# Performance work log

Measured on AMD Instinct MI355X. Metric: run time of the kernel, lower is better.

## Reference

```python
import jax, jax.numpy as jnp
import numpy as np

B, NL, C, H, W = 4, 2048, 128, 128, 128
N_PTS0, N_PTS1 = 32, 8
SCALE = N_PTS0 // N_PTS1  # MaxPool1d kernel/stride
FEATURE_DIM = 5
BN_EPS = 1e-5


def setup_inputs() -> dict:
    key = jax.random.key(0)
    ks = jax.random.split(key, 12)
    fm = jax.random.normal(ks[0], (B, C, H, W), dtype=jnp.float32)
    lines = jax.random.uniform(ks[1], (B, NL, 2, 2), dtype=jnp.float32) * 128.0
    P = C // 2
    s = 0.05
    return {
        "feature_map": fm,
        "lines": lines,
        # Bottleneck1D params (BatchNorm in eval mode: running_mean=0, running_var=1)
        "bn1_g": jnp.ones((C,), jnp.float32), "bn1_b": jnp.zeros((C,), jnp.float32),
        "conv1_w": jax.random.normal(ks[2], (P, C, 1), jnp.float32) * s,
        "conv1_b": jnp.zeros((P,), jnp.float32),
        "bn2_g": jnp.ones((P,), jnp.float32), "bn2_b": jnp.zeros((P,), jnp.float32),
        "conv2_w": jax.random.normal(ks[3], (P, P, 3), jnp.float32) * s,
        "conv2_b": jnp.zeros((P,), jnp.float32),
        "bn3_g": jnp.ones((P,), jnp.float32), "bn3_b": jnp.zeros((P,), jnp.float32),
        "conv3_w": jax.random.normal(ks[4], (C, P, 1), jnp.float32) * s,
        "conv3_b": jnp.zeros((C,), jnp.float32),
        # fc2: ReLU -> Linear(dim_loi*n_pts1 + 5, 4)
        "fc2_w": jax.random.normal(ks[5], (4, C * N_PTS1 + FEATURE_DIM), jnp.float32) * s,
        "fc2_b": jnp.zeros((4,), jnp.float32),
    }


def _bn(x, g, b):
    # eval-mode BatchNorm1d with running_mean=0, running_var=1
    return x * (g / jnp.sqrt(1.0 + BN_EPS))[None, :, None] + b[None, :, None]


def _conv1d(x, w, b, pad):
    y = jax.lax.conv_general_dilated(x, w, (1,), [(pad, pad)],
                                     dimension_numbers=("NCH", "OIH", "NCH"))
    return y + b[None, :, None]


def _loi_gather(fm, lines):
    # sample points along each line: [B, NL, N_PTS0, 2]
    lam = jnp.linspace(0.0, 1.0, N_PTS0, dtype=jnp.float32)[None, None, :, None]
    p = lines[:, :, 0:1, :] * lam + lines[:, :, 1:2, :] * (1.0 - lam) - 0.5
    p = p.reshape(B, -1, 2)                      # [B, NL*N_PTS0, 2]
    px, py = p[..., 0], p[..., 1]
    px0 = jnp.clip(jnp.floor(px), 0.0, 127.0)
    py0 = jnp.clip(jnp.floor(py), 0.0, 127.0)
    px1 = jnp.clip(px0 + 1.0, 0.0, 127.0)
    py1 = jnp.clip(py0 + 1.0, 0.0, 127.0)
    px0l, py0l = px0.astype(jnp.int32), py0.astype(jnp.int32)
    px1l, py1l = px1.astype(jnp.int32), py1.astype(jnp.int32)

    gather = jax.vmap(lambda f, yi, xi: f[:, yi, xi])  # [C, P] per image
    # weights exactly as in the torch source
    xp = (gather(fm, py0l, px0l) * ((px1 - px) * (py1 - py))[:, None, :]
          + gather(fm, py1l, px0l) * ((px - px0) * (py1 - py))[:, None, :]
          + gather(fm, py0l, px1l) * ((px1 - px) * (py - py0))[:, None, :]
          + gather(fm, py1l, px1l) * ((px - px0) * (py - py0))[:, None, :])
    # [B, C, NL*N_PTS0] -> [B*NL, C, N_PTS0]
    xp = xp.reshape(B, C, NL, N_PTS0).transpose(0, 2, 1, 3).reshape(B * NL, C, N_PTS0)
    return xp


def reference(feature_map, lines, bn1_g, bn1_b, conv1_w, conv1_b,
              bn2_g, bn2_b, conv2_w, conv2_b, bn3_g, bn3_b,
              conv3_w, conv3_b, fc2_w, fc2_b):
    xp = _loi_gather(feature_map, lines)               # [B*NL, C, N_PTS0]
    # MaxPool1d(SCALE, SCALE)
    x = xp.reshape(B * NL, C, N_PTS1, SCALE).max(axis=-1)
    # Bottleneck1D residual block
    y = jax.nn.relu(_bn(x, bn1_g, bn1_b))
    y = _conv1d(y, conv1_w, conv1_b, 0)
    y = jax.nn.relu(_bn(y, bn2_g, bn2_b))
    y = _conv1d(y, conv2_w, conv2_b, 1)
    y = jax.nn.relu(_bn(y, bn3_g, bn3_b))
    y = _conv1d(y, conv3_w, conv3_b, 0)
    x = x + y                                          # [B*NL, C, N_PTS1]
    # line geometry feature (use_cood=1, use_slop=1)
    xyu, xyv = lines[:, :, 0, :], lines[:, :, 1, :]
    u2v = jnp.sqrt(((xyu - xyv) ** 2).sum(-1, keepdims=True)).clip(min=1e-6)
    f = jnp.concatenate([xyu / 128.0, xyv / 128.0, u2v], axis=-1)
    f = f.reshape(B * NL, FEATURE_DIM)
    # concat + fc2 (ReLU -> Linear)
    x = jnp.concatenate([x.reshape(B * NL, C * N_PTS1), f], axis=1)
    logits = jax.nn.relu(x) @ fc2_w.T + fc2_b
    prob = jax.nn.softmax(logits, axis=1)
    return logits, prob
```

## Files before the change

### kernel.cpp

```cpp
#include <hip/hip_runtime.h>
#include <math.h>

#define BB 4
#define NLL 2048
#define CC 128
#define HH 128
#define WW 128
#define NPTS0 32
#define NPTS1 8
#define PP 64
#define FDIM 5
#define FCK (CC*NPTS1 + FDIM)
#define FCKP 1032

typedef __attribute__((ext_vector_type(8))) short bf16x8;
typedef __attribute__((ext_vector_type(4))) float f32x4;

__device__ __forceinline__ unsigned short f2bf(float f) {
    union { float f; unsigned u; } v; v.f = f;
    unsigned u = v.u;
    return (unsigned short)((u + 0x7fffu + ((u >> 16) & 1u)) >> 16);
}
__device__ __forceinline__ float bf2f(unsigned short s) {
    union { unsigned u; float f; } v; v.u = ((unsigned)s) << 16;
    return v.f;
}

__global__ __launch_bounds__(256)
void transpose_prep(const float* __restrict__ fm, const float* __restrict__ w1,
                    const float* __restrict__ w2, const float* __restrict__ w3,
                    const float* __restrict__ fcw,
                    unsigned short* __restrict__ fmT,
                    unsigned short* __restrict__ W1b,
                    unsigned short* __restrict__ W2b,
                    unsigned short* __restrict__ W3b,
                    float* __restrict__ fcwP) {
    const int t = threadIdx.x;
    if (blockIdx.x >= 512) {
        int gid = (blockIdx.x - 512) * 256 + t;
        for (int e = gid; e < 32800; e += 4096) {
            if (e < 8192) {
                W1b[e] = f2bf(w1[e]);
            } else if (e < 20480) {
                int g = e - 8192;
                int tt = g >> 12, r = g & 4095;
                int p = r >> 6, q = r & 63;
                W2b[tt * 4096 + p * 64 + q] = f2bf(w2[p * 192 + q * 3 + tt]);
            } else if (e < 28672) {
                int g = e - 20480;
                W3b[g] = f2bf(w3[g]);
            } else {
                int g = e - 28672;
                int o = g / FCKP, r = g - o * FCKP;
                fcwP[g] = (r < FCK) ? fcw[o * FCK + r] : 0.0f;
            }
        }
        return;
    }
    __shared__ unsigned short tile[2][128 * 72];
    const int by = blockIdx.x;
    const int b = by >> 7, y = by & 127;
    const float* src = fm + ((size_t)b * CC) * (HH * WW) + (size_t)y * WW;
    const int x4 = (t & 31) * 4;
    const int xh = x4 >> 6, xl = x4 & 63;
    #pragma unroll
    for (int i = 0; i < 16; ++i) {
        int r = (t >> 5) + 8 * i;
        float4 v = *(const float4*)&src[(size_t)r * (HH * WW) + x4];
        ushort4 u;
        u.x = f2bf(v.x); u.y = f2bf(v.y); u.z = f2bf(v.z); u.w = f2bf(v.w);
        *(ushort4*)&tile[xh][r * 72 + (xl ^ (r & 28))] = u;
    }
    __syncthreads();
    const int c4 = (t & 31) * 4;
    #pragma unroll
    for (int h = 0; h < 2; ++h) {
        unsigned short* dst = fmT + ((size_t)by * WW + h * 64) * CC;
        #pragma unroll
        for (int i = 0; i < 8; ++i) {
            int x = (t >> 5) + 8 * i;
            ushort4 u;
            u.x = tile[h][(c4 + 0) * 72 + (x ^ ((c4 + 0) & 28))];
            u.y = tile[h][(c4 + 1) * 72 + (x ^ ((c4 + 1) & 28))];
            u.z = tile[h][(c4 + 2) * 72 + (x ^ ((c4 + 2) & 28))];
            u.w = tile[h][(c4 + 3) * 72 + (x ^ ((c4 + 3) & 28))];
            *(ushort4*)&dst[(size_t)x * CC + c4] = u;
        }
    }
}

__global__ __launch_bounds__(256, 8)
void line_mfma(const unsigned short* __restrict__ fmT,
               const float* __restrict__ lines,
               const float* __restrict__ bn1_g, const float* __restrict__ bn1_b,
               const unsigned short* __restrict__ W1b, const float* __restrict__ b1,
               const float* __restrict__ bn2_g, const float* __restrict__ bn2_b,
               const unsigned short* __restrict__ W2b, const float* __restrict__ b2,
               const float* __restrict__ bn3_g, const float* __restrict__ bn3_b,
               const unsigned short* __restrict__ W3b, const float* __restrict__ b3,
               const float* __restrict__ fcwP,  const float* __restrict__ fcb,
               float* __restrict__ out) {
    __shared__ int   s_oA[64], s_oB[64], s_oC[64], s_oD[64];
    __shared__ float s_wA[64], s_wB[64], s_wC[64], s_wD[64];
    __shared__ float s_xs[16 * 132];
    __shared__ unsigned short s_ybn[16 * 136];
    __shared__ unsigned short s_z1[2 * 10 * 72];
    __shared__ unsigned short s_z2[16 * 72];
    __shared__ float s_feat[2][8];
    __shared__ float s_red[4 * 8];

    const int bx  = blockIdx.x;
    const int L0  = bx * 2;
    const int b   = bx >> 10;
    const int tid = threadIdx.x;
    const int lane = tid & 63;
    const int wv   = tid >> 6;
    const int quad = lane >> 4;
    const int l16  = lane & 15;
    const float inv_s = 1.0f / sqrtf(1.0f + 1e-5f);

    if (tid < 64) {
        int line = tid >> 5, pt = tid & 31;
        const float* ln = lines + (size_t)(L0 + line) * 4;
        float lam = (float)pt * (1.0f / 31.0f);
        float om  = 1.0f - lam;
        float px = ln[0] * lam + ln[2] * om - 0.5f;
        float py = ln[1] * lam + ln[3] * om - 0.5f;
        float px0 = fminf(fmaxf(floorf(px), 0.0f), 127.0f);
        float py0 = fminf(fmaxf(floorf(py), 0.0f), 127.0f);
        float px1 = fminf(px0 + 1.0f, 127.0f);
        float py1 = fminf(py0 + 1.0f, 127.0f);
        int ix0 = (int)px0, ix1 = (int)px1, iy0 = (int)py0, iy1 = (int)py1;
        s_oA[tid] = (iy0 * WW + ix0) * CC;
        s_oB[tid] = (iy1 * WW + ix0) * CC;
        s_oC[tid] = (iy0 * WW + ix1) * CC;
        s_oD[tid] = (iy1 * WW + ix1) * CC;
        float ax = px1 - px, bxv = px - px0, ay = py1 - py, byv = py - py0;
        s_wA[tid] = ax  * ay;
        s_wB[tid] = bxv * ay;
        s_wC[tid] = ax  * byv;
        s_wD[tid] = bxv * byv;
    }
    if (tid >= 64 && tid < 66) {
        int line = tid - 64;
        const float* ln = lines + (size_t)(L0 + line) * 4;
        float ux = ln[0], uy = ln[1], vx = ln[2], vy = ln[3];
        float dx = ux - vx, dy = uy - vy;
        float d = fmaxf(sqrtf(dx * dx + dy * dy), 1e-6f);
        s_feat[line][0] = ux * (1.0f / 128.0f);
        s_feat[line][1] = uy * (1.0f / 128.0f);
        s_feat[line][2] = vx * (1.0f / 128.0f);
        s_feat[line][3] = vy * (1.0f / 128.0f);
        s_feat[line][4] = d;
    }
    if (tid < 128) {
        int line = tid >> 6, q = tid & 63;
        s_z1[line * 720 + 0 * 72 + q] = 0;
        s_z1[line * 720 + 9 * 72 + q] = 0;
    }
    __syncthreads();

    {
        int tl = tid >> 4;
        int line = tl >> 3, k = tl & 7;
        int c8 = (tid & 15) * 8;
        const unsigned short* base = fmT + (size_t)b * (HH * WW * CC) + c8;
        float acc[8];
        #pragma unroll
        for (int i = 0; i < 8; ++i) acc[i] = -INFINITY;
        #pragma unroll
        for (int j = 0; j < 4; ++j) {
            int pt = line * 32 + k * 4 + j;
            bf16x8 rA = *(const bf16x8*)(base + s_oA[pt]);
            bf16x8 rB = *(const bf16x8*)(base + s_oB[pt]);
            bf16x8 rC = *(const bf16x8*)(base + s_oC[pt]);
            bf16x8 rD = *(const bf16x8*)(base + s_oD[pt]);
            float wA = s_wA[pt], wB = s_wB[pt], wC = s_wC[pt], wD = s_wD[pt];
            #pragma unroll
            for (int i = 0; i < 8; ++i) {
                float v = wA * bf2f((unsigned short)rA[i])
                        + wB * bf2f((unsigned short)rB[i])
                        + wC * bf2f((unsigned short)rC[i])
                        + wD * bf2f((unsigned short)rD[i]);
                acc[i] = fmaxf(acc[i], v);
            }
        }
        float* xr = &s_xs[tl * 132 + c8];
        f32x4 lo = {acc[0], acc[1], acc[2], acc[3]};
        f32x4 hi = {acc[4], acc[5], acc[6], acc[7]};
        *(f32x4*)&xr[0] = lo;
        *(f32x4*)&xr[4] = hi;
        bf16x8 pack;
        #pragma unroll
        for (int i = 0; i < 8; ++i) {
            float v = fmaxf(acc[i] * (bn1_g[c8 + i] * inv_s) + bn1_b[c8 + i], 0.0f);
            pack[i] = (short)f2bf(v);
        }
        *(bf16x8*)&s_ybn[tl * 136 + c8] = pack;
    }
    __syncthreads();

    {
        int n0 = wv * 16;
        f32x4 acc = {0.f, 0.f, 0.f, 0.f};
        #pragma unroll
        for (int kc = 0; kc < 4; ++kc) {
            bf16x8 a = *(const bf16x8*)&s_ybn[l16 * 136 + kc * 32 + quad * 8];
            bf16x8 bf = *(const bf16x8*)(W1b + (n0 + l16) * 128 + kc * 32 + quad * 8);
            acc = __builtin_amdgcn_mfma_f32_16x16x32_bf16(a, bf, acc, 0, 0, 0);
        }
        int p = n0 + l16;
        float s2 = bn2_g[p] * inv_s, bb2 = bn2_b[p], cb = b1[p];
        int line = quad >> 1;
        int kbase = (quad & 1) * 4;
        #pragma unroll
        for (int r = 0; r < 4; ++r) {
            float v = fmaxf((acc[r] + cb) * s2 + bb2, 0.0f);
            s_z1[line * 720 + (kbase + r + 1) * 72 + p] = f2bf(v);
        }
    }
    __syncthreads();

    {
        int n0 = wv * 16;
        f32x4 acc = {0.f, 0.f, 0.f, 0.f};
        int line = l16 >> 3, k = l16 & 7;
        #pragma unroll
        for (int t = 0; t < 3; ++t) {
            const unsigned short* arow = &s_z1[line * 720 + (k + t) * 72];
            #pragma unroll
            for (int kc = 0; kc < 2; ++kc) {
                bf16x8 a = *(const bf16x8*)&arow[kc * 32 + quad * 8];
                bf16x8 bf = *(const bf16x8*)(W2b + t * 4096 + (n0 + l16) * 64 + kc * 32 + quad * 8);
                acc = __builtin_amdgcn_mfma_f32_16x16x32_bf16(a, bf, acc, 0, 0, 0);
            }
        }
        int p = n0 + l16;
        float s3 = bn3_g[p] * inv_s, bb3 = bn3_b[p], cb = b2[p];
        #pragma unroll
        for (int r = 0; r < 4; ++r) {
            float v = fmaxf((acc[r] + cb) * s3 + bb3, 0.0f);
            s_z2[(quad * 4 + r) * 72 + p] = f2bf(v);
        }
    }
    __syncthreads();

    float p0 = 0.f, p1 = 0.f, p2 = 0.f, p3 = 0.f;
    {
        int kbase = (quad & 1) * 4;
        bf16x8 a0 = *(const bf16x8*)&s_z2[l16 * 72 + 0 * 32 + quad * 8];
        bf16x8 a1 = *(const bf16x8*)&s_z2[l16 * 72 + 1 * 32 + quad * 8];
        #pragma unroll
        for (int sub = 0; sub < 2; ++sub) {
            int n0 = wv * 32 + sub * 16;
            f32x4 acc = {0.f, 0.f, 0.f, 0.f};
            bf16x8 bf0 = *(const bf16x8*)(W3b + (n0 + l16) * 64 + 0 * 32 + quad * 8);
            bf16x8 bf1 = *(const bf16x8*)(W3b + (n0 + l16) * 64 + 1 * 32 + quad * 8);
            acc = __builtin_amdgcn_mfma_f32_16x16x32_bf16(a0, bf0, acc, 0, 0, 0);
            acc = __builtin_amdgcn_mfma_f32_16x16x32_bf16(a1, bf1, acc, 0, 0, 0);
            int c = n0 + l16;
            float cb = b3[c];
            int idx = c * 8 + kbase;
            float4 w0 = *(const float4*)(fcwP + 0 * FCKP + idx);
            float4 w1v = *(const float4*)(fcwP + 1 * FCKP + idx);
            float4 w2v = *(const float4*)(fcwP + 2 * FCKP + idx);
            float4 w3v = *(const float4*)(fcwP + 3 * FCKP + idx);
            const float* w0a = (const float*)&w0;
            const float* w1a = (const float*)&w1v;
            const float* w2a = (const float*)&w2v;
            const float* w3a = (const float*)&w3v;
            #pragma unroll
            for (int r = 0; r < 4; ++r) {
                int m = quad * 4 + r;
                float v = fmaxf(s_xs[m * 132 + c] + acc[r] + cb, 0.0f);
                p0 = fmaf(v, w0a[r], p0);
                p1 = fmaf(v, w1a[r], p1);
                p2 = fmaf(v, w2a[r], p2);
                p3 = fmaf(v, w3a[r], p3);
            }
        }
    }
    #pragma unroll
    for (int off = 16; off >= 1; off >>= 1) {
        p0 += __shfl_down(p0, off);
        p1 += __shfl_down(p1, off);
        p2 += __shfl_down(p2, off);
        p3 += __shfl_down(p3, off);
    }
    if ((lane & 31) == 0) {
        int line = lane >> 5;
        s_red[wv * 8 + line * 4 + 0] = p0;
        s_red[wv * 8 + line * 4 + 1] = p1;
        s_red[wv * 8 + line * 4 + 2] = p2;
        s_red[wv * 8 + line * 4 + 3] = p3;
    }
    __syncthreads();

    if (tid < 2) {
        int line = tid;
        float lg[4];
        #pragma unroll
        for (int o = 0; o < 4; ++o) {
            lg[o] = fcb[o] + s_red[0 + line * 4 + o] + s_red[8 + line * 4 + o]
                  + s_red[16 + line * 4 + o] + s_red[24 + line * 4 + o];
        }
        #pragma unroll
        for (int j = 0; j < FDIM; ++j) {
            float fv = fmaxf(s_feat[line][j], 0.0f);
            #pragma unroll
            for (int o = 0; o < 4; ++o)
                lg[o] = fmaf(fv, fcwP[o * FCKP + 1024 + j], lg[o]);
        }
        float m = fmaxf(fmaxf(lg[0], lg[1]), fmaxf(lg[2], lg[3]));
        float e0 = expf(lg[0] - m), e1 = expf(lg[1] - m);
        float e2 = expf(lg[2] - m), e3 = expf(lg[3] - m);
        float inv = 1.0f / (e0 + e1 + e2 + e3);
        float* lo = out + (size_t)(L0 + line) * 4;
        lo[0] = lg[0]; lo[1] = lg[1]; lo[2] = lg[2]; lo[3] = lg[3];
        float* pr = out + (size_t)BB * NLL * 4 + (size_t)(L0 + line) * 4;
        pr[0] = e0 * inv; pr[1] = e1 * inv; pr[2] = e2 * inv; pr[3] = e3 * inv;
    }
}

__global__ __launch_bounds__(256)
void transpose_fm2(const float* __restrict__ fm, float* __restrict__ fmT) {
    __shared__ float tile[32 * 132];
    const int c0 = blockIdx.x * 32;
    const int by = blockIdx.y;
    const int b = by >> 7, y = by & 127;
    const int t = threadIdx.x;
    const float* src = fm + ((size_t)b * CC) * (HH * WW) + (size_t)y * WW;
    const int x4 = (t & 31) * 4;
    #pragma unroll
    for (int i = 0; i < 4; ++i) {
        int r = (t >> 5) + 8 * i;
        *(float4*)&tile[r * 132 + x4] =
            *(const float4*)&src[(size_t)(c0 + r) * (HH * WW) + x4];
    }
    __syncthreads();
    float* dst = fmT + (size_t)by * WW * CC + c0 + (t & 31);
    const int cr = (t & 31) * 132;
    #pragma unroll
    for (int i = 0; i < 16; ++i) {
        int x = (t >> 5) + 8 * i;
        dst[(size_t)x * CC] = tile[cr + x];
    }
}

template<bool TRANS>
__global__ __launch_bounds__(256)
void line_kernel_v1(const float* __restrict__ fm,
                    const float* __restrict__ lines,
                    const float* __restrict__ bn1_g, const float* __restrict__ bn1_b,
                    const float* __restrict__ w1,    const float* __restrict__ b1,
                    const float* __restrict__ bn2_g, const float* __restrict__ bn2_b,
                    const float* __restrict__ w2,    const float* __restrict__ b2,
                    const float* __restrict__ bn3_g, const float* __restrict__ bn3_b,
                    const float* __restrict__ w3,    const float* __restrict__ b3,
                    const float* __restrict__ fcw,   const float* __restrict__ fcb,
                    float* __restrict__ out) {
    __shared__ int   s_ix0[32], s_ix1[32], s_iy0[32], s_iy1[32];
    __shared__ float s_wA[32], s_wB[32], s_wC[32], s_wD[32];
    __shared__ float xs [8][132];
    __shared__ float ybn[8][132];
    __shared__ float z1 [64][12];
    __shared__ float z2 [64][8];
    __shared__ float s_feat[8];
    __shared__ float s_red[16];

    const int L   = blockIdx.x;
    const int b   = L / NLL;
    const int tid = threadIdx.x;
    const float inv_s = 1.0f / sqrtf(1.0f + 1e-5f);
    const float* ln = lines + (size_t)L * 4;

    if (tid < 32) {
        float lam = (float)tid * (1.0f / 31.0f);
        float om  = 1.0f - lam;
        float px = ln[0] * lam + ln[2] * om - 0.5f;
        float py = ln[1] * lam + ln[3] * om - 0.5f;
        float px0 = fminf(fmaxf(floorf(px), 0.0f), 127.0f);
        float py0 = fminf(fmaxf(floorf(py), 0.0f), 127.0f);
        float px1 = fminf(px0 + 1.0f, 127.0f);
        float py1 = fminf(py0 + 1.0f, 127.0f);
        s_ix0[tid] = (int)px0; s_ix1[tid] = (int)px1;
        s_iy0[tid] = (int)py0; s_iy1[tid] = (int)py1;
        float ax = px1 - px, bxv = px - px0, ay = py1 - py, byv = py - py0;
        s_wA[tid] = ax  * ay;  s_wB[tid] = bxv * ay;
        s_wC[tid] = ax  * byv; s_wD[tid] = bxv * byv;
    }
    if (tid == 0) {
        float ux = ln[0], uy = ln[1], vx = ln[2], vy = ln[3];
        float dx = ux - vx, dy = uy - vy;
        float d = fmaxf(sqrtf(dx * dx + dy * dy), 1e-6f);
        s_feat[0] = ux / 128.0f; s_feat[1] = uy / 128.0f;
        s_feat[2] = vx / 128.0f; s_feat[3] = vy / 128.0f;
        s_feat[4] = d;
    }
    __syncthreads();
    {
        int cq = tid & 31, k = tid >> 5, c0 = cq * 4;
        float4 acc;
        acc.x = -INFINITY; acc.y = -INFINITY; acc.z = -INFINITY; acc.w = -INFINITY;
        #pragma unroll
        for (int j = 0; j < 4; ++j) {
            int pt = k * 4 + j;
            int ix0 = s_ix0[pt], ix1 = s_ix1[pt];
            int iy0 = s_iy0[pt], iy1 = s_iy1[pt];
            float wA = s_wA[pt], wB = s_wB[pt], wC = s_wC[pt], wD = s_wD[pt];
            float4 vA, vB, vC, vD;
            if (TRANS) {
                const float* base = fm + (size_t)b * HH * WW * CC;
                vA = *(const float4*)(base + ((size_t)(iy0 * WW + ix0)) * CC + c0);
                vB = *(const float4*)(base + ((size_t)(iy1 * WW + ix0)) * CC + c0);
                vC = *(const float4*)(base + ((size_t)(iy0 * WW + ix1)) * CC + c0);
                vD = *(const float4*)(base + ((size_t)(iy1 * WW + ix1)) * CC + c0);
            } else {
                const float* base = fm + ((size_t)b * CC + c0) * HH * WW;
                int oA = iy0 * WW + ix0, oB = iy1 * WW + ix0;
                int oC = iy0 * WW + ix1, oD = iy1 * WW + ix1;
                vA.x = base[oA];           vB.x = base[oB];
                vC.x = base[oC];           vD.x = base[oD];
                vA.y = base[HH*WW + oA];   vB.y = base[HH*WW + oB];
                vC.y = base[HH*WW + oC];   vD.y = base[HH*WW + oD];
                vA.z = base[2*HH*WW + oA]; vB.z = base[2*HH*WW + oB];
                vC.z = base[2*HH*WW + oC]; vD.z = base[2*HH*WW + oD];
                vA.w = base[3*HH*WW + oA]; vB.w = base[3*HH*WW + oB];
                vC.w = base[3*HH*WW + oC]; vD.w = base[3*HH*WW + oD];
            }
            float4 v;
            v.x = wA * vA.x + wB * vB.x + wC * vC.x + wD * vD.x;
            v.y = wA * vA.y + wB * vB.y + wC * vC.y + wD * vD.y;
            v.z = wA * vA.z + wB * vB.z + wC * vC.z + wD * vD.z;
            v.w = wA * vA.w + wB * vB.w + wC * vC.w + wD * vD.w;
            acc.x = fmaxf(acc.x, v.x); acc.y = fmaxf(acc.y, v.y);
            acc.z = fmaxf(acc.z, v.z); acc.w = fmaxf(acc.w, v.w);
        }
        *(float4*)(&xs[k][c0]) = acc;
    }
    __syncthreads();
    for (int e = tid; e < 1024; e += 256) {
        int k = e >> 7, c = e & 127;
        ybn[k][c] = fmaxf(xs[k][c] * (bn1_g[c] * inv_s) + bn1_b[c], 0.0f);
    }
    __syncthreads();
    if (tid < 64) { z1[tid][0] = 0.0f; z1[tid][9] = 0.0f; }
    {
        int p = tid >> 2, kq = tid & 3;
        const float* wrow = w1 + p * 128;
        float a0a = 0.f, a0b = 0.f, a1a = 0.f, a1b = 0.f;
        #pragma unroll 8
        for (int c = 0; c < 128; c += 4) {
            float4 w  = *(const float4*)(wrow + c);
            float4 ya = *(const float4*)(&ybn[kq][c]);
            float4 yb = *(const float4*)(&ybn[kq + 4][c]);
            a0a = fmaf(w.x, ya.x, a0a); a0b = fmaf(w.y, ya.y, a0b);
            a0a = fmaf(w.z, ya.z, a0a); a0b = fmaf(w.w, ya.w, a0b);
            a1a = fmaf(w.x, yb.x, a1a); a1b = fmaf(w.y, yb.y, a1b);
            a1a = fmaf(w.z, yb.z, a1a); a1b = fmaf(w.w, yb.w, a1b);
        }
        float s2 = bn2_g[p] * inv_s, bb = bn2_b[p], cb = b1[p];
        z1[p][1 + kq]     = fmaxf((a0a + a0b + cb) * s2 + bb, 0.0f);
        z1[p][1 + kq + 4] = fmaxf((a1a + a1b + cb) * s2 + bb, 0.0f);
    }
    __syncthreads();
    {
        int p = tid >> 2, kq = tid & 3;
        const float* wrow = w2 + p * 192;
        float acc0 = 0.f, acc1 = 0.f;
        #pragma unroll 4
        for (int q = 0; q < 64; ++q) {
            float w0 = wrow[q * 3 + 0], w1v = wrow[q * 3 + 1], w2v = wrow[q * 3 + 2];
            const float* zr = &z1[q][0];
            acc0 = fmaf(w0, zr[kq], acc0);
            acc0 = fmaf(w1v, zr[kq + 1], acc0);
            acc0 = fmaf(w2v, zr[kq + 2], acc0);
            acc1 = fmaf(w0, zr[kq + 4], acc1);
            acc1 = fmaf(w1v, zr[kq + 5], acc1);
            acc1 = fmaf(w2v, zr[kq + 6], acc1);
        }
        float s3 = bn3_g[p] * inv_s, bb = bn3_b[p], cb = b2[p];
        z2[p][kq]     = fmaxf((acc0 + cb) * s3 + bb, 0.0f);
        z2[p][kq + 4] = fmaxf((acc1 + cb) * s3 + bb, 0.0f);
    }
    __syncthreads();
    float part0 = 0.f, part1 = 0.f, part2 = 0.f, part3 = 0.f;
    {
        int c = tid >> 1, kq = tid & 1;
        const float* wrow = w3 + c * 64;
        float acc[4] = {0.f, 0.f, 0.f, 0.f};
        #pragma unroll 8
        for (int q = 0; q < 64; ++q) {
            float w = wrow[q];
            acc[0] = fmaf(w, z2[q][kq], acc[0]);
            acc[1] = fmaf(w, z2[q][kq + 2], acc[1]);
            acc[2] = fmaf(w, z2[q][kq + 4], acc[2]);
            acc[3] = fmaf(w, z2[q][kq + 6], acc[3]);
        }
        float cb = b3[c];
        #pragma unroll
        for (int i = 0; i < 4; ++i) {
            int k = kq + 2 * i;
            float v = fmaxf(xs[k][c] + acc[i] + cb, 0.0f);
            int idx = c * 8 + k;
            part0 = fmaf(v, fcw[0 * FCK + idx], part0);
            part1 = fmaf(v, fcw[1 * FCK + idx], part1);
            part2 = fmaf(v, fcw[2 * FCK + idx], part2);
            part3 = fmaf(v, fcw[3 * FCK + idx], part3);
        }
    }
    #pragma unroll
    for (int off = 32; off > 0; off >>= 1) {
        part0 += __shfl_down(part0, off);
        part1 += __shfl_down(part1, off);
        part2 += __shfl_down(part2, off);
        part3 += __shfl_down(part3, off);
    }
    if ((tid & 63) == 0) {
        int w = tid >> 6;
        s_red[w * 4 + 0] = part0; s_red[w * 4 + 1] = part1;
        s_red[w * 4 + 2] = part2; s_red[w * 4 + 3] = part3;
    }
    __syncthreads();
    if (tid == 0) {
        float lg[4];
        #pragma unroll
        for (int o = 0; o < 4; ++o)
            lg[o] = fcb[o] + s_red[o] + s_red[4 + o] + s_red[8 + o] + s_red[12 + o];
        #pragma unroll
        for (int j = 0; j < FDIM; ++j) {
            float fv = fmaxf(s_feat[j], 0.0f);
            #pragma unroll
            for (int o = 0; o < 4; ++o)
                lg[o] = fmaf(fv, fcw[o * FCK + 1024 + j], lg[o]);
        }
        float m = fmaxf(fmaxf(lg[0], lg[1]), fmaxf(lg[2], lg[3]));
        float e0 = expf(lg[0] - m), e1 = expf(lg[1] - m);
        float e2 = expf(lg[2] - m), e3 = expf(lg[3] - m);
        float inv = 1.0f / (e0 + e1 + e2 + e3);
        float* lo = out + (size_t)L * 4;
        lo[0] = lg[0]; lo[1] = lg[1]; lo[2] = lg[2]; lo[3] = lg[3];
        float* pr = out + (size_t)BB * NLL * 4 + (size_t)L * 4;
        pr[0] = e0 * inv; pr[1] = e1 * inv; pr[2] = e2 * inv; pr[3] = e3 * inv;
    }
}

extern "C" void kernel_launch(void* const* d_in, const int* in_sizes, int n_in,
                              void* d_out, int out_size, void* d_ws, size_t ws_size,
                              hipStream_t stream) {
    const float* fm     = (const float*)d_in[0];
    const float* lines  = (const float*)d_in[1];
    const float* bn1_g  = (const float*)d_in[2];
    const float* bn1_b  = (const float*)d_in[3];
    const float* w1     = (const float*)d_in[4];
    const float* b1     = (const float*)d_in[5];
    const float* bn2_g  = (const float*)d_in[6];
    const float* bn2_b  = (const float*)d_in[7];
    const float* w2     = (const float*)d_in[8];
    const float* b2     = (const float*)d_in[9];
    const float* bn3_g  = (const float*)d_in[10];
    const float* bn3_b  = (const float*)d_in[11];
    const float* w3     = (const float*)d_in[12];
    const float* b3     = (const float*)d_in[13];
    const float* fcw    = (const float*)d_in[14];
    const float* fcb    = (const float*)d_in[15];
    float* out = (float*)d_out;

    const size_t fmTb_bytes = (size_t)BB * HH * WW * CC * sizeof(unsigned short);
    const size_t fmTf_bytes = (size_t)BB * HH * WW * CC * sizeof(float);
    const size_t wb_bytes   = 57344;
    const size_t fcwP_bytes = 4 * FCKP * sizeof(float);

    if (ws_size >= fmTb_bytes + wb_bytes + fcwP_bytes) {
        unsigned short* fmT = (unsigned short*)d_ws;
        unsigned short* W1b = (unsigned short*)((char*)d_ws + fmTb_bytes);
        unsigned short* W2b = W1b + 8192;
        unsigned short* W3b = W2b + 12288;
        float* fcwP = (float*)((char*)d_ws + fmTb_bytes + wb_bytes);
        transpose_prep<<<512 + 16, 256, 0, stream>>>(
            fm, w1, w2, w3, fcw, fmT, W1b, W2b, W3b, fcwP);
        line_mfma<<<BB * NLL / 2, 256, 0, stream>>>(
            fmT, lines, bn1_g, bn1_b, W1b, b1, bn2_g, bn2_b, W2b, b2,
            bn3_g, bn3_b, W3b, b3, fcwP, fcb, out);
    } else if (ws_size >= fmTf_bytes) {
        float* fmT = (float*)d_ws;
        dim3 tg(CC / 32, BB * HH);
        transpose_fm2<<<tg, 256, 0, stream>>>(fm, fmT);
        line_kernel_v1<true><<<BB * NLL, 256, 0, stream>>>(
            fmT, lines, bn1_g, bn1_b, w1, b1, bn2_g, bn2_b, w2, b2,
            bn3_g, bn3_b, w3, b3, fcw, fcb, out);
    } else {
        line_kernel_v1<false><<<BB * NLL, 256, 0, stream>>>(
            fm, lines, bn1_g, bn1_b, w1, b1, bn2_g, bn2_b, w2, b2,
            bn3_g, bn3_b, w3, b3, fcw, fcb, out);
    }
}
```

Baseline: 152.1 us.

## Split transpose into half-row blocks and hoist all gather loads before compute

```diff
diff --git a/kernel.cpp b/kernel.cpp
--- a/kernel.cpp
+++ b/kernel.cpp
@@ -36,8 +36,8 @@
                     unsigned short* __restrict__ W3b,
                     float* __restrict__ fcwP) {
     const int t = threadIdx.x;
-    if (blockIdx.x >= 512) {
-        int gid = (blockIdx.x - 512) * 256 + t;
+    if (blockIdx.x >= 1024) {
+        int gid = (blockIdx.x - 1024) * 256 + t;
         for (int e = gid; e < 32800; e += 4096) {
             if (e < 8192) {
                 W1b[e] = f2bf(w1[e]);
@@ -57,39 +57,37 @@
         }
         return;
     }
-    __shared__ unsigned short tile[2][128 * 72];
-    const int by = blockIdx.x;
+    __shared__ unsigned short tile[128 * 72];
+    const int bh = blockIdx.x;
+    const int by = bh >> 1;
+    const int h  = bh & 1;
     const int b = by >> 7, y = by & 127;
-    const float* src = fm + ((size_t)b * CC) * (HH * WW) + (size_t)y * WW;
-    const int x4 = (t & 31) * 4;
-    const int xh = x4 >> 6, xl = x4 & 63;
+    const float* src = fm + ((size_t)b * CC) * (HH * WW) + (size_t)y * WW + h * 64;
+    const int x4 = (t & 15) * 4;
     #pragma unroll
-    for (int i = 0; i < 16; ++i) {
-        int r = (t >> 5) + 8 * i;
+    for (int i = 0; i < 8; ++i) {
+        int r = (t >> 4) + 16 * i;
         float4 v = *(const float4*)&src[(size_t)r * (HH * WW) + x4];
         ushort4 u;
         u.x = f2bf(v.x); u.y = f2bf(v.y); u.z = f2bf(v.z); u.w = f2bf(v.w);
-        *(ushort4*)&tile[xh][r * 72 + (xl ^ (r & 28))] = u;
+        *(ushort4*)&tile[r * 72 + (x4 ^ (r & 28))] = u;
     }
     __syncthreads();
     const int c4 = (t & 31) * 4;
+    unsigned short* dst = fmT + ((size_t)by * WW + h * 64) * CC;
     #pragma unroll
-    for (int h = 0; h < 2; ++h) {
-        unsigned short* dst = fmT + ((size_t)by * WW + h * 64) * CC;
-        #pragma unroll
-        for (int i = 0; i < 8; ++i) {
-            int x = (t >> 5) + 8 * i;
-            ushort4 u;
-            u.x = tile[h][(c4 + 0) * 72 + (x ^ ((c4 + 0) & 28))];
-            u.y = tile[h][(c4 + 1) * 72 + (x ^ ((c4 + 1) & 28))];
-            u.z = tile[h][(c4 + 2) * 72 + (x ^ ((c4 + 2) & 28))];
-            u.w = tile[h][(c4 + 3) * 72 + (x ^ ((c4 + 3) & 28))];
-            *(ushort4*)&dst[(size_t)x * CC + c4] = u;
-        }
+    for (int i = 0; i < 8; ++i) {
+        int x = (t >> 5) + 8 * i;
+        ushort4 u;
+        u.x = tile[(c4 + 0) * 72 + (x ^ ((c4 + 0) & 28))];
+        u.y = tile[(c4 + 1) * 72 + (x ^ ((c4 + 1) & 28))];
+        u.z = tile[(c4 + 2) * 72 + (x ^ ((c4 + 2) & 28))];
+        u.w = tile[(c4 + 3) * 72 + (x ^ ((c4 + 3) & 28))];
+        *(ushort4*)&dst[(size_t)x * CC + c4] = u;
     }
 }
 
-__global__ __launch_bounds__(256, 8)
+__global__ __launch_bounds__(256, 5)
 void line_mfma(const unsigned short* __restrict__ fmT,
                const float* __restrict__ lines,
                const float* __restrict__ bn1_g, const float* __restrict__ bn1_b,
@@ -165,23 +163,28 @@
         int line = tl >> 3, k = tl & 7;
         int c8 = (tid & 15) * 8;
         const unsigned short* base = fmT + (size_t)b * (HH * WW * CC) + c8;
+        const int pt0 = line * 32 + k * 4;
+        bf16x8 rA[4], rB[4], rC[4], rD[4];
+        #pragma unroll
+        for (int j = 0; j < 4; ++j) {
+            rA[j] = *(const bf16x8*)(base + s_oA[pt0 + j]);
+            rB[j] = *(const bf16x8*)(base + s_oB[pt0 + j]);
+            rC[j] = *(const bf16x8*)(base + s_oC[pt0 + j]);
+            rD[j] = *(const bf16x8*)(base + s_oD[pt0 + j]);
+        }
         float acc[8];
         #pragma unroll
         for (int i = 0; i < 8; ++i) acc[i] = -INFINITY;
         #pragma unroll
         for (int j = 0; j < 4; ++j) {
-            int pt = line * 32 + k * 4 + j;
-            bf16x8 rA = *(const bf16x8*)(base + s_oA[pt]);
-            bf16x8 rB = *(const bf16x8*)(base + s_oB[pt]);
-            bf16x8 rC = *(const bf16x8*)(base + s_oC[pt]);
-            bf16x8 rD = *(const bf16x8*)(base + s_oD[pt]);
+            int pt = pt0 + j;
             float wA = s_wA[pt], wB = s_wB[pt], wC = s_wC[pt], wD = s_wD[pt];
             #pragma unroll
             for (int i = 0; i < 8; ++i) {
-                float v = wA * bf2f((unsigned short)rA[i])
-                        + wB * bf2f((unsigned short)rB[i])
-                        + wC * bf2f((unsigned short)rC[i])
-                        + wD * bf2f((unsigned short)rD[i]);
+                float v = wA * bf2f((unsigned short)rA[j][i])
+                        + wB * bf2f((unsigned short)rB[j][i])
+                        + wC * bf2f((unsigned short)rC[j][i])
+                        + wD * bf2f((unsigned short)rD[j][i]);
                 acc[i] = fmaxf(acc[i], v);
             }
         }
@@ -577,7 +580,7 @@
         unsigned short* W2b = W1b + 8192;
         unsigned short* W3b = W2b + 12288;
         float* fcwP = (float*)((char*)d_ws + fmTb_bytes + wb_bytes);
-        transpose_prep<<<512 + 16, 256, 0, stream>>>(
+        transpose_prep<<<1024 + 16, 256, 0, stream>>>(
             fm, w1, w2, w3, fcw, fmT, W1b, W2b, W3b, fcwP);
         line_mfma<<<BB * NLL / 2, 256, 0, stream>>>(
             fmT, lines, bn1_g, bn1_b, W1b, b1, bn2_g, bn2_b, W2b, b2,
```

After: 152.2 us. Within noise of the previous version (+0.1%).
